# Optimization experiments

Hardware: AMD Instinct MI355X
Metric: run time of the kernel (lower is better)

The kernel has to match this reference:

```python
import jax, jax.numpy as jnp
import numpy as np

N, E, B, T = 50000, 800000, 256, 50
IN_DIM, H, C1, C2, Q_DIM, LH = 128, 4, 32, 128, 32, 128
EPS = 1e-5


def setup_inputs() -> dict:
    key = jax.random.key(0)
    ks = jax.random.split(key, 24)
    g = 0.05
    inp = {
        'x': jax.random.normal(ks[0], (N, IN_DIM), jnp.float32),
        'edge_index': jax.random.randint(ks[1], (2, E), 0, N, jnp.int32),
        'batch': jnp.sort(jax.random.randint(ks[2], (N,), 0, B, jnp.int32)),
        'quant': jax.random.normal(ks[3], (B, T, Q_DIM), jnp.float32),
        # GATConv(128 -> 32, heads=4, concat)
        'gat_W': jax.random.normal(ks[4], (IN_DIM, H * C1), jnp.float32) * g,
        'gat_att_src': jax.random.normal(ks[5], (H, C1), jnp.float32) * g,
        'gat_att_dst': jax.random.normal(ks[6], (H, C1), jnp.float32) * g,
        'gat_b': jnp.zeros((H * C1,), jnp.float32),
        # BN1 over 128 channels (eval mode)
        'bn1_gamma': jnp.ones((H * C1,), jnp.float32),
        'bn1_beta': jnp.zeros((H * C1,), jnp.float32),
        'bn1_mean': jax.random.normal(ks[7], (H * C1,), jnp.float32) * 0.01,
        'bn1_var': jnp.ones((H * C1,), jnp.float32),
        # GCNConv(128 -> 128)
        'gcn_W': jax.random.normal(ks[8], (H * C1, C2), jnp.float32) * g,
        'gcn_b': jnp.zeros((C2,), jnp.float32),
        'bn2_gamma': jnp.ones((C2,), jnp.float32),
        'bn2_beta': jnp.zeros((C2,), jnp.float32),
        'bn2_mean': jax.random.normal(ks[9], (C2,), jnp.float32) * 0.01,
        'bn2_var': jnp.ones((C2,), jnp.float32),
        # GlobalAttention gate: Linear(C2 -> 1)
        'gate_W': jax.random.normal(ks[10], (1, C2), jnp.float32) * g,
        'gate_b': jnp.zeros((1,), jnp.float32),
        # LSTM(Q_DIM -> LH), torch gate order i,f,g,o
        'lstm_Wih': jax.random.normal(ks[11], (4 * LH, Q_DIM), jnp.float32) * g,
        'lstm_Whh': jax.random.normal(ks[12], (4 * LH, LH), jnp.float32) * g,
        'lstm_bih': jnp.zeros((4 * LH,), jnp.float32),
        'lstm_bhh': jnp.zeros((4 * LH,), jnp.float32),
        # final Linear(C2+LH -> 1)
        'fc_W': jax.random.normal(ks[13], (1, C2 + LH), jnp.float32) * g,
        'fc_b': jnp.zeros((1,), jnp.float32),
    }
    return inp


def _segment_softmax(e, seg, num_segments):
    m = jax.ops.segment_max(e, seg, num_segments=num_segments)
    ex = jnp.exp(e - m[seg])
    s = jax.ops.segment_sum(ex, seg, num_segments=num_segments)
    return ex / (s[seg] + 1e-16)


def _bn_eval(x, gamma, beta, mean, var):
    return gamma * (x - mean) * jax.lax.rsqrt(var + EPS) + beta


def _forward(x, edge_index, batch, quant,
             gat_W, gat_att_src, gat_att_dst, gat_b,
             bn1_gamma, bn1_beta, bn1_mean, bn1_var,
             gcn_W, gcn_b, bn2_gamma, bn2_beta, bn2_mean, bn2_var,
             gate_W, gate_b,
             lstm_Wih, lstm_Whh, lstm_bih, lstm_bhh,
             fc_W, fc_b):
    n = x.shape[0]
    loops = jnp.arange(n, dtype=edge_index.dtype)
    ei = jnp.concatenate([edge_index, jnp.stack([loops, loops])], axis=1)  # add self loops
    src, dst = ei[0], ei[1]

    # ---- GATConv ----
    xw = (x @ gat_W).reshape(n, H, C1)                      # [N,H,C1]
    a_src = jnp.sum(xw * gat_att_src, axis=-1)              # [N,H]
    a_dst = jnp.sum(xw * gat_att_dst, axis=-1)
    e = jax.nn.leaky_relu(a_src[src] + a_dst[dst], 0.2)     # [E+N,H]
    alpha = _segment_softmax(e, dst, n)                     # softmax over in-edges per dst
    msg = xw[src] * alpha[:, :, None]                       # [E+N,H,C1]
    h = jax.ops.segment_sum(msg, dst, num_segments=n).reshape(n, H * C1) + gat_b

    h = jax.nn.elu(h)
    h = _bn_eval(h, bn1_gamma, bn1_beta, bn1_mean, bn1_var)

    # ---- GCNConv (sym-normalized with self loops) ----
    deg = jax.ops.segment_sum(jnp.ones_like(dst, jnp.float32), dst, num_segments=n)
    dinv = jnp.where(deg > 0, jax.lax.rsqrt(deg), 0.0)
    norm = dinv[src] * dinv[dst]                            # [E+N]
    hw = h @ gcn_W                                          # [N,C2]
    h2 = jax.ops.segment_sum(hw[src] * norm[:, None], dst, num_segments=n) + gcn_b

    h2 = jax.nn.elu(h2)
    h2 = _bn_eval(h2, bn2_gamma, bn2_beta, bn2_mean, bn2_var)

    # ---- GlobalAttention pooling over graphs ----
    gate = (h2 @ gate_W.T + gate_b)[:, 0]                   # [N]
    score = _segment_softmax(gate, batch, B)
    graph_rep = jax.ops.segment_sum(score[:, None] * h2, batch, num_segments=B)  # [B,C2]

    # ---- LSTM over quant series ----
    def step(carry, xt):
        hh, cc = carry
        gates = xt @ lstm_Wih.T + hh @ lstm_Whh.T + lstm_bih + lstm_bhh
        i, f, gg, o = jnp.split(gates, 4, axis=-1)
        cc = jax.nn.sigmoid(f) * cc + jax.nn.sigmoid(i) * jnp.tanh(gg)
        hh = jax.nn.sigmoid(o) * jnp.tanh(cc)
        return (hh, cc), None

    h0 = jnp.zeros((B, LH), quant.dtype)
    (hT, _), _ = jax.lax.scan(step, (h0, h0), jnp.swapaxes(quant, 0, 1))

    combined = jnp.concatenate([graph_rep, hT], axis=1)     # [B, C2+LH]
    out = (combined @ fc_W.T + fc_b)[:, 0]                  # [B]
    return out


def reference(x, edge_index, batch, quant,
              gat_W, gat_att_src, gat_att_dst, gat_b,
              bn1_gamma, bn1_beta, bn1_mean, bn1_var,
              gcn_W, gcn_b, bn2_gamma, bn2_beta, bn2_mean, bn2_var,
              gate_W, gate_b,
              lstm_Wih, lstm_Whh, lstm_bih, lstm_bhh,
              fc_W, fc_b):
    return _forward(x, edge_index, batch, quant,
                    gat_W, gat_att_src, gat_att_dst, gat_b,
                    bn1_gamma, bn1_beta, bn1_mean, bn1_var,
                    gcn_W, gcn_b, bn2_gamma, bn2_beta, bn2_mean, bn2_var,
                    gate_W, gate_b,
                    lstm_Wih, lstm_Whh, lstm_bih, lstm_bhh,
                    fc_W, fc_b)
```

## Files before the change

### kernel.cpp

```cpp
#include <hip/hip_runtime.h>
#include <cfloat>
#include <cstddef>

constexpr int KIN   = 128;
constexpr int KQD   = 32;
constexpr int KT    = 50;
constexpr int KLH   = 128;
constexpr float BN_EPS = 1e-5f;

typedef __attribute__((ext_vector_type(8))) short bf16x8;
typedef __attribute__((ext_vector_type(4))) float f32x4;
union U8 { bf16x8 v; unsigned u[4]; };

__device__ __forceinline__ float elu_f(float x)  { return x > 0.f ? x : expm1f(x); }
__device__ __forceinline__ float leaky_f(float x){ return x > 0.f ? x : 0.2f * x; }
__device__ __forceinline__ float fsigm(float x)  { return 1.f / (1.f + __expf(-x)); }
__device__ __forceinline__ float ftanh(float x)  { return 1.f - 2.f / (__expf(2.f * x) + 1.f); }

__device__ __forceinline__ unsigned bfpack(float lo, float hi) {
    unsigned ul = __float_as_uint(lo), uh = __float_as_uint(hi);
    ul += 0x7FFFu + ((ul >> 16) & 1u);
    uh += 0x7FFFu + ((uh >> 16) & 1u);
    return (ul >> 16) | (uh & 0xFFFF0000u);
}
__device__ __forceinline__ unsigned short bf1(float v) {
    unsigned u = __float_as_uint(v);
    u += 0x7FFFu + ((u >> 16) & 1u);
    return (unsigned short)(u >> 16);
}
__device__ __forceinline__ float bflo(unsigned u) { return __uint_as_float(u << 16); }
__device__ __forceinline__ float bfhi(unsigned u) { return __uint_as_float(u & 0xFFFF0000u); }

__device__ __forceinline__ bf16x8 pack8(float4 p, float4 q) {
    U8 t;
    t.u[0] = bfpack(p.x, p.y); t.u[1] = bfpack(p.z, p.w);
    t.u[2] = bfpack(q.x, q.y); t.u[3] = bfpack(q.z, q.w);
    return t.v;
}

__global__ void k_deg(const int* __restrict__ ei, int E, int* __restrict__ deg) {
    int e = blockIdx.x * blockDim.x + threadIdx.x;
    if (e < E) atomicAdd(&deg[ei[E + e]], 1);
}

__global__ __launch_bounds__(1024)
void k_scan_a(const int* __restrict__ deg, int n, int* __restrict__ bsum) {
    __shared__ int wsum[16];
    int tid = threadIdx.x, lane = tid & 63, w = tid >> 6;
    int i0 = blockIdx.x * 4096 + tid * 4;
    int t = 0;
    #pragma unroll
    for (int j = 0; j < 4; j++) t += (i0 + j < n) ? deg[i0 + j] : 0;
    #pragma unroll
    for (int d = 1; d < 64; d <<= 1) t += __shfl_xor(t, d);
    if (lane == 0) wsum[w] = t;
    __syncthreads();
    if (tid == 0) {
        int s = 0;
        #pragma unroll
        for (int k = 0; k < 16; k++) s += wsum[k];
        bsum[blockIdx.x] = s;
    }
}

__global__ void k_scan_b(int* __restrict__ bsum, int nb) {
    if (threadIdx.x == 0) {
        int run = 0;
        for (int i = 0; i < nb; i++) { int v = bsum[i]; bsum[i] = run; run += v; }
    }
}

__global__ __launch_bounds__(1024)
void k_scan_c(const int* __restrict__ deg, int n, const int* __restrict__ bsum,
              int* __restrict__ offsets, int* __restrict__ cursor,
              float* __restrict__ dinv) {
    __shared__ int wsum[16];
    int tid = threadIdx.x, lane = tid & 63, w = tid >> 6;
    int i0 = blockIdx.x * 4096 + tid * 4;
    int v[4];
    #pragma unroll
    for (int j = 0; j < 4; j++) v[j] = (i0 + j < n) ? deg[i0 + j] : 0;
    int tsum = v[0] + v[1] + v[2] + v[3];
    int sc = tsum;
    #pragma unroll
    for (int d = 1; d < 64; d <<= 1) {
        int o = __shfl_up(sc, d);
        if (lane >= d) sc += o;
    }
    if (lane == 63) wsum[w] = sc;
    __syncthreads();
    if (w == 0) {
        int xx = (lane < 16) ? wsum[lane] : 0;
        #pragma unroll
        for (int d = 1; d < 16; d <<= 1) {
            int o = __shfl_up(xx, d);
            if (lane >= d) xx += o;
        }
        if (lane < 16) wsum[lane] = xx;
    }
    __syncthreads();
    int run = bsum[blockIdx.x] + ((w > 0) ? wsum[w - 1] : 0) + sc - tsum;
    #pragma unroll
    for (int j = 0; j < 4; j++) {
        int i = i0 + j;
        if (i < n) {
            cursor[i]      = run;
            offsets[i + 1] = run + v[j];
            dinv[i]        = rsqrtf((float)(v[j] + 1));
            run += v[j];
        }
    }
    if (blockIdx.x == 0 && tid == 0) offsets[0] = 0;
}

__global__ void k_fill(const int* __restrict__ ei, int E, int* __restrict__ cursor,
                       int* __restrict__ csr_src) {
    int e = blockIdx.x * blockDim.x + threadIdx.x;
    if (e < E) {
        int s = ei[e], d = ei[E + e];
        int pos = atomicAdd(&cursor[d], 1);
        csr_src[pos] = s;
    }
}

template <bool ATT>
__global__ __launch_bounds__(256, 4)
void k_gemm_mfma(const float* __restrict__ X, const float* __restrict__ W,
                 unsigned* __restrict__ Yb, int nrows,
                 const float* __restrict__ attS, const float* __restrict__ attD,
                 float* __restrict__ a_src, float* __restrict__ a_dst) {
    __shared__ float tile[16][132];
    __shared__ float as_sh[128], ad_sh[128];
    int tid  = threadIdx.x;
    int lane = tid & 63;
    int wv   = tid >> 6;
    if (ATT && tid < 128) { as_sh[tid] = attS[tid]; ad_sh[tid] = attD[tid]; }
    int l16 = lane & 15;
    int kq  = (lane >> 4) * 8;
    bf16x8 bfr[2][4];
    #pragma unroll
    for (int nt = 0; nt < 2; nt++) {
        int n = wv * 32 + nt * 16 + l16;
        #pragma unroll
        for (int kk = 0; kk < 4; kk++) {
            int k0 = kk * 32 + kq;
            float f[8];
            #pragma unroll
            for (int j = 0; j < 8; j++) f[j] = W[(size_t)(k0 + j) * 128 + n];
            U8 t;
            t.u[0] = bfpack(f[0], f[1]); t.u[1] = bfpack(f[2], f[3]);
            t.u[2] = bfpack(f[4], f[5]); t.u[3] = bfpack(f[6], f[7]);
            bfr[nt][kk] = t.v;
        }
    }
    int nch = (nrows + 15) / 16;
    for (int ch = blockIdx.x; ch < nch; ch += gridDim.x) {
        int r0 = ch * 16;
        int r  = r0 + l16;
        bool rok = r < nrows;
        const float* xr = X + (size_t)r * 128 + kq;
        float4 z4 = make_float4(0.f, 0.f, 0.f, 0.f);
        bf16x8 afr[4];
        #pragma unroll
        for (int kk = 0; kk < 4; kk++) {
            float4 p = rok ? *reinterpret_cast<const float4*>(xr + kk * 32)     : z4;
            float4 q = rok ? *reinterpret_cast<const float4*>(xr + kk * 32 + 4) : z4;
            afr[kk] = pack8(p, q);
        }
        f32x4 acc0 = {0.f, 0.f, 0.f, 0.f};
        f32x4 acc1 = {0.f, 0.f, 0.f, 0.f};
        #pragma unroll
        for (int kk = 0; kk < 4; kk++) {
            acc0 = __builtin_amdgcn_mfma_f32_16x16x32_bf16(afr[kk], bfr[0][kk], acc0, 0, 0, 0);
            acc1 = __builtin_amdgcn_mfma_f32_16x16x32_bf16(afr[kk], bfr[1][kk], acc1, 0, 0, 0);
        }
        __syncthreads();
        int rowb = (lane >> 4) * 4;
        int cb   = wv * 32 + l16;
        #pragma unroll
        for (int reg = 0; reg < 4; reg++) {
            tile[rowb + reg][cb]      = acc0[reg];
            tile[rowb + reg][cb + 16] = acc1[reg];
        }
        __syncthreads();
        #pragma unroll
        for (int i = 0; i < 4; i++) {
            int idx = tid + i * 256;
            int row = idx >> 6, cp = idx & 63;
            int rr = r0 + row;
            if (rr < nrows) {
                float2 f = *reinterpret_cast<const float2*>(&tile[row][cp * 2]);
                Yb[(size_t)rr * 64 + cp] = bfpack(f.x, f.y);
            }
        }
        if (ATT && tid < 64) {
            int rr2 = tid >> 2, h = tid & 3;
            if (r0 + rr2 < nrows) {
                float ps = 0.f, pd = 0.f;
                #pragma unroll
                for (int j = 0; j < 32; j++) {
                    float v = tile[rr2][h * 32 + j];
                    ps += v * as_sh[h * 32 + j];
                    pd += v * ad_sh[h * 32 + j];
                }
                a_src[(size_t)(r0 + rr2) * 4 + h] = ps;
                a_dst[(size_t)(r0 + rr2) * 4 + h] = pd;
            }
        }
    }
}

__global__ __launch_bounds__(256)
void k_gat_agg(const int* __restrict__ offsets, const int* __restrict__ csr_src,
               const float* __restrict__ a_src, const float* __restrict__ a_dst,
               const unsigned* __restrict__ xwb, const float* __restrict__ bias,
               const float* __restrict__ g1, const float* __restrict__ b1,
               const float* __restrict__ mu1, const float* __restrict__ var1,
               float* __restrict__ hout, int n) {
    __shared__ int   src_sh[4][64];
    __shared__ float al_sh[4][4][64];
    int lane = threadIdx.x & 63;
    int wv   = threadIdx.x >> 6;
    int wid  = (blockIdx.x * blockDim.x + threadIdx.x) >> 6;
    int nw   = (gridDim.x * blockDim.x) >> 6;
    int hP   = lane >> 4;
    int c0 = lane * 2, c1 = c0 + 1;
    float bi0 = bias[c0], bi1 = bias[c1];
    float A0 = g1[c0] * rsqrtf(var1[c0] + BN_EPS);
    float A1 = g1[c1] * rsqrtf(var1[c1] + BN_EPS);
    float B0 = b1[c0] - mu1[c0] * A0;
    float B1 = b1[c1] - mu1[c1] * A1;
    for (int node = wid; node < n; node += nw) {
        int beg = offsets[node], end = offsets[node + 1];
        int rowlen = end - beg, total = rowlen + 1;
        float4 adv = *reinterpret_cast<const float4*>(&a_dst[(size_t)node * 4]);
        int sv = (lane < rowlen) ? csr_src[beg + lane] : node;
        float4 as4 = *reinterpret_cast<const float4*>(&a_src[(size_t)sv * 4]);
        float e0 = leaky_f(as4.x + adv.x), e1 = leaky_f(as4.y + adv.y);
        float e2 = leaky_f(as4.z + adv.z), e3 = leaky_f(as4.w + adv.w);
        float m[4] = {-FLT_MAX, -FLT_MAX, -FLT_MAX, -FLT_MAX};
        if (lane < total) { m[0] = e0; m[1] = e1; m[2] = e2; m[3] = e3; }
        for (int i = lane + 64; i < total; i += 64) {
            int src = (i < rowlen) ? csr_src[beg + i] : node;
            float4 a4 = *reinterpret_cast<const float4*>(&a_src[(size_t)src * 4]);
            m[0] = fmaxf(m[0], leaky_f(a4.x + adv.x));
            m[1] = fmaxf(m[1], leaky_f(a4.y + adv.y));
            m[2] = fmaxf(m[2], leaky_f(a4.z + adv.z));
            m[3] = fmaxf(m[3], leaky_f(a4.w + adv.w));
        }
        #pragma unroll
        for (int off = 32; off; off >>= 1) {
            #pragma unroll
            for (int h = 0; h < 4; h++) m[h] = fmaxf(m[h], __shfl_xor(m[h], off));
        }
        float ex[4] = {0.f, 0.f, 0.f, 0.f};
        if (lane < total) {
            ex[0] = expf(e0 - m[0]); ex[1] = expf(e1 - m[1]);
            ex[2] = expf(e2 - m[2]); ex[3] = expf(e3 - m[3]);
        }
        float s[4] = {ex[0], ex[1], ex[2], ex[3]};
        for (int i = lane + 64; i < total; i += 64) {
            int src = (i < rowlen) ? csr_src[beg + i] : node;
            float4 a4 = *reinterpret_cast<const float4*>(&a_src[(size_t)src * 4]);
            s[0] += expf(leaky_f(a4.x + adv.x) - m[0]);
            s[1] += expf(leaky_f(a4.y + adv.y) - m[1]);
            s[2] += expf(leaky_f(a4.z + adv.z) - m[2]);
            s[3] += expf(leaky_f(a4.w + adv.w) - m[3]);
        }
        #pragma unroll
        for (int off = 32; off; off >>= 1) {
            #pragma unroll
            for (int h = 0; h < 4; h++) s[h] += __shfl_xor(s[h], off);
        }
        float inv[4];
        #pragma unroll
        for (int h = 0; h < 4; h++) inv[h] = 1.f / (s[h] + 1e-16f);
        src_sh[wv][lane] = sv;
        #pragma unroll
        for (int h = 0; h < 4; h++) al_sh[wv][h][lane] = ex[h] * inv[h];
        __builtin_amdgcn_wave_barrier();
        float acc0 = 0.f, acc1 = 0.f;
        int cnt = min(total, 64);
        {
            int i = 0;
            for (; i + 4 <= cnt; i += 4) {
                int s0 = src_sh[wv][i],     s1 = src_sh[wv][i + 1];
                int s2 = src_sh[wv][i + 2], s3 = src_sh[wv][i + 3];
                float a0 = al_sh[wv][hP][i],     a1 = al_sh[wv][hP][i + 1];
                float a2 = al_sh[wv][hP][i + 2], a3 = al_sh[wv][hP][i + 3];
                unsigned u0 = xwb[(size_t)s0 * 64 + lane];
                unsigned u1 = xwb[(size_t)s1 * 64 + lane];
                unsigned u2 = xwb[(size_t)s2 * 64 + lane];
                unsigned u3 = xwb[(size_t)s3 * 64 + lane];
                acc0 += a0 * bflo(u0); acc1 += a0 * bfhi(u0);
                acc0 += a1 * bflo(u1); acc1 += a1 * bfhi(u1);
                acc0 += a2 * bflo(u2); acc1 += a2 * bfhi(u2);
                acc0 += a3 * bflo(u3); acc1 += a3 * bfhi(u3);
            }
            for (; i < cnt; i++) {
                int src  = src_sh[wv][i];
                float aP = al_sh[wv][hP][i];
                unsigned u = xwb[(size_t)src * 64 + lane];
                acc0 += aP * bflo(u);
                acc1 += aP * bfhi(u);
            }
        }
        for (int base = 64; base < total; base += 64) {
            __builtin_amdgcn_wave_barrier();
            int i = base + lane;
            int src2 = node;
            float a0v = 0.f, a1v = 0.f, a2v = 0.f, a3v = 0.f;
            if (i < total) {
                if (i < rowlen) src2 = csr_src[beg + i];
                float4 a4 = *reinterpret_cast<const float4*>(&a_src[(size_t)src2 * 4]);
                a0v = expf(leaky_f(a4.x + adv.x) - m[0]) * inv[0];
                a1v = expf(leaky_f(a4.y + adv.y) - m[1]) * inv[1];
                a2v = expf(leaky_f(a4.z + adv.z) - m[2]) * inv[2];
                a3v = expf(leaky_f(a4.w + adv.w) - m[3]) * inv[3];
            }
            src_sh[wv][lane] = src2;
            al_sh[wv][0][lane] = a0v; al_sh[wv][1][lane] = a1v;
            al_sh[wv][2][lane] = a2v; al_sh[wv][3][lane] = a3v;
            __builtin_amdgcn_wave_barrier();
            int cnt2 = min(total - base, 64);
            for (int j = 0; j < cnt2; j++) {
                int src  = src_sh[wv][j];
                float aP = al_sh[wv][hP][j];
                unsigned u = xwb[(size_t)src * 64 + lane];
                acc0 += aP * bflo(u);
                acc1 += aP * bfhi(u);
            }
        }
        __builtin_amdgcn_wave_barrier();
        float vA = elu_f(acc0 + bi0);
        float vB = elu_f(acc1 + bi1);
        vA = vA * A0 + B0;
        vB = vB * A1 + B1;
        *reinterpret_cast<float2*>(&hout[(size_t)node * 128 + c0]) =
            make_float2(vA, vB);
    }
}

__global__ __launch_bounds__(256)
void k_gcn_agg(const int* __restrict__ offsets, const int* __restrict__ csr_src,
               const float* __restrict__ dinv, const unsigned* __restrict__ hwb,
               const float* __restrict__ bias,
               const float* __restrict__ g2, const float* __restrict__ b2,
               const float* __restrict__ mu2, const float* __restrict__ var2,
               const float* __restrict__ gateW, const float* __restrict__ gateB,
               float* __restrict__ h2, float* __restrict__ gate, int n) {
    __shared__ int   src_sh[4][64];
    __shared__ float w_sh[4][64];
    int lane = threadIdx.x & 63;
    int wv   = threadIdx.x >> 6;
    int wid  = (blockIdx.x * blockDim.x + threadIdx.x) >> 6;
    int nw   = (gridDim.x * blockDim.x) >> 6;
    int c0 = lane * 2, c1 = c0 + 1;
    float bi0 = bias[c0], bi1 = bias[c1];
    float A0 = g2[c0] * rsqrtf(var2[c0] + BN_EPS);
    float A1 = g2[c1] * rsqrtf(var2[c1] + BN_EPS);
    float B0 = b2[c0] - mu2[c0] * A0;
    float B1 = b2[c1] - mu2[c1] * A1;
    float gw0 = gateW[c0], gw1 = gateW[c1], gB = gateB[0];
    for (int node = wid; node < n; node += nw) {
        int beg = offsets[node], end = offsets[node + 1];
        int rowlen = end - beg;
        float dn = dinv[node];
        unsigned us = hwb[(size_t)node * 64 + lane];
        float acc0 = dn * dn * bflo(us);
        float acc1 = dn * dn * bfhi(us);
        for (int base = 0; base < rowlen; base += 64) {
            __builtin_amdgcn_wave_barrier();
            int i = base + lane;
            int src2 = node;
            float wv2 = 0.f;
            if (i < rowlen) { src2 = csr_src[beg + i]; wv2 = dinv[src2] * dn; }
            src_sh[wv][lane] = src2;
            w_sh[wv][lane]   = wv2;
            __builtin_amdgcn_wave_barrier();
            int cnt = min(rowlen - base, 64);
            int j = 0;
            for (; j + 4 <= cnt; j += 4) {
                int s0 = src_sh[wv][j],     s1 = src_sh[wv][j + 1];
                int s2 = src_sh[wv][j + 2], s3 = src_sh[wv][j + 3];
                float w0 = w_sh[wv][j],     w1 = w_sh[wv][j + 1];
                float w2 = w_sh[wv][j + 2], w3 = w_sh[wv][j + 3];
                unsigned u0 = hwb[(size_t)s0 * 64 + lane];
                unsigned u1 = hwb[(size_t)s1 * 64 + lane];
                unsigned u2 = hwb[(size_t)s2 * 64 + lane];
                unsigned u3 = hwb[(size_t)s3 * 64 + lane];
                acc0 += w0 * bflo(u0); acc1 += w0 * bfhi(u0);
                acc0 += w1 * bflo(u1); acc1 += w1 * bfhi(u1);
                acc0 += w2 * bflo(u2); acc1 += w2 * bfhi(u2);
                acc0 += w3 * bflo(u3); acc1 += w3 * bfhi(u3);
            }
            for (; j < cnt; j++) {
                int src = src_sh[wv][j];
                float w = w_sh[wv][j];
                unsigned u = hwb[(size_t)src * 64 + lane];
                acc0 += w * bflo(u);
                acc1 += w * bfhi(u);
            }
        }
        __builtin_amdgcn_wave_barrier();
        float vA = elu_f(acc0 + bi0);
        float vB = elu_f(acc1 + bi1);
        vA = vA * A0 + B0;
        vB = vB * A1 + B1;
        *reinterpret_cast<float2*>(&h2[(size_t)node * 128 + c0]) =
            make_float2(vA, vB);
        float p = vA * gw0 + vB * gw1;
        #pragma unroll
        for (int off = 32; off; off >>= 1) p += __shfl_xor(p, off);
        if (lane == 0) gate[node] = p + gB;
    }
}

__device__ __forceinline__ int lbound(const int* a, int n, int key) {
    int lo = 0, hi = n;
    while (lo < hi) { int mid = (lo + hi) >> 1; if (a[mid] < key) lo = mid + 1; else hi = mid; }
    return lo;
}

__global__ __launch_bounds__(256)
void k_pool(const int* __restrict__ batch, const float* __restrict__ gate,
            const float* __restrict__ h2, const float* __restrict__ hT,
            const float* __restrict__ fcW, const float* __restrict__ fcB,
            float* __restrict__ out, int n) {
    int b = blockIdx.x, tid = threadIdx.x;
    __shared__ float red[256];
    __shared__ float sc_sh[256];
    int start = lbound(batch, n, b);
    int end   = lbound(batch, n, b + 1);
    float m = -FLT_MAX;
    for (int i = start + tid; i < end; i += 256) m = fmaxf(m, gate[i]);
    red[tid] = m; __syncthreads();
    for (int s2 = 128; s2 > 0; s2 >>= 1) {
        if (tid < s2) red[tid] = fmaxf(red[tid], red[tid + s2]);
        __syncthreads();
    }
    m = red[0]; __syncthreads();
    float s = 0.f;
    for (int i = start + tid; i < end; i += 256) s += expf(gate[i] - m);
    red[tid] = s; __syncthreads();
    for (int s2 = 128; s2 > 0; s2 >>= 1) {
        if (tid < s2) red[tid] += red[tid + s2];
        __syncthreads();
    }
    float inv = 1.f / (red[0] + 1e-16f);
    __syncthreads();
    int j = tid & 127, half = tid >> 7;
    float acc = 0.f;
    for (int base = start; base < end; base += 256) {
        int cnt = min(256, end - base);
        __syncthreads();
        if (tid < cnt) sc_sh[tid] = expf(gate[base + tid] - m) * inv;
        __syncthreads();
        for (int ii = half; ii < cnt; ii += 2)
            acc += sc_sh[ii] * h2[(size_t)(base + ii) * 128 + j];
    }
    red[tid] = acc; __syncthreads();
    if (half == 0) sc_sh[j] = red[j] + red[128 + j];
    __syncthreads();
    float p = 0.f;
    if (tid < 128)
        p = fcW[tid] * sc_sh[tid] + fcW[128 + tid] * hT[(size_t)b * 128 + tid];
    red[tid] = p; __syncthreads();
    for (int s2 = 128; s2 > 0; s2 >>= 1) {
        if (tid < s2) red[tid] += red[tid + s2];
        __syncthreads();
    }
    if (tid == 0) out[b] = red[0] + fcB[0];
}

__global__ __launch_bounds__(256)
void k_xproj(const float* __restrict__ quant, const float* __restrict__ Wih,
             const float* __restrict__ bih, const float* __restrict__ bhh,
             float* __restrict__ xproj) {
    int blk = blockIdx.x;
    int chunk = blk / KT, s = blk % KT;
    int lane = threadIdx.x & 63, w = threadIdx.x >> 6;
    int l15 = lane & 15, kq8 = (lane >> 4) * 8;
    int b = chunk * 16 + l15;
    const float* xr = &quant[(size_t)b * (KT * KQD) + s * KQD + kq8];
    bf16x8 ax = pack8(*reinterpret_cast<const float4*>(xr),
                      *reinterpret_cast<const float4*>(xr + 4));
    #pragma unroll
    for (int ti = 0; ti < 8; ti++) {
        int tc = w * 8 + ti;
        int gcol = w * 128 + ti * 16 + l15;
        const float* wr = &Wih[(size_t)gcol * KQD + kq8];
        bf16x8 bw = pack8(*reinterpret_cast<const float4*>(wr),
                          *reinterpret_cast<const float4*>(wr + 4));
        f32x4 acc = {0.f, 0.f, 0.f, 0.f};
        acc = __builtin_amdgcn_mfma_f32_16x16x32_bf16(ax, bw, acc, 0, 0, 0);
        float bv = bih[gcol] + bhh[gcol];
        acc[0] += bv; acc[1] += bv; acc[2] += bv; acc[3] += bv;
        *reinterpret_cast<f32x4*>(
            &xproj[(((size_t)chunk * KT + s) * 32 + tc) * 256 + lane * 4]) = acc;
    }
}

__global__ __launch_bounds__(512)
void k_lstm2(const float* __restrict__ xproj, const float* __restrict__ Whh,
             float* __restrict__ hstate) {
    __shared__ unsigned short h16[2][16][148];
    int t = threadIdx.x, lane = t & 63, w = t >> 6;
    int chunk = blockIdx.x;
    int l15 = lane & 15, kq8 = (lane >> 4) * 8;
    int j = w * 16 + l15;
    int rowq = (lane >> 4) * 4;
    bf16x8 whh_f[4][4];
    #pragma unroll
    for (int c = 0; c < 4; c++) {
        int col = c * 128 + j;
        #pragma unroll
        for (int kk = 0; kk < 4; kk++) {
            const float* wr = &Whh[(size_t)col * 128 + kk * 32 + kq8];
            whh_f[c][kk] = pack8(*reinterpret_cast<const float4*>(wr),
                                 *reinterpret_cast<const float4*>(wr + 4));
        }
    }
    for (int p = t; p < 16 * 148; p += 512) {
        int r = p / 148, cc = p - r * 148;
        h16[0][r][cc] = 0;
    }
    float cst[4] = {0.f, 0.f, 0.f, 0.f};
    const float* xb = xproj + ((size_t)chunk * KT) * 32 * 256;
    f32x4 xgA = *reinterpret_cast<const f32x4*>(&xb[(0 * 8 + w) * 256 + lane * 4]);
    f32x4 xgB = *reinterpret_cast<const f32x4*>(&xb[(1 * 8 + w) * 256 + lane * 4]);
    f32x4 xgC = *reinterpret_cast<const f32x4*>(&xb[(2 * 8 + w) * 256 + lane * 4]);
    f32x4 xgD = *reinterpret_cast<const f32x4*>(&xb[(3 * 8 + w) * 256 + lane * 4]);
    int cur = 0;
    __syncthreads();
    for (int s = 0; s < KT; s++) {
        f32x4 ai = xgA, af = xgB, ag = xgC, ao = xgD;
        #pragma unroll
        for (int kk = 0; kk < 4; kk++) {
            bf16x8 ah = *reinterpret_cast<const bf16x8*>(&h16[cur][l15][kk * 32 + kq8]);
            ai = __builtin_amdgcn_mfma_f32_16x16x32_bf16(ah, whh_f[0][kk], ai, 0, 0, 0);
            af = __builtin_amdgcn_mfma_f32_16x16x32_bf16(ah, whh_f[1][kk], af, 0, 0, 0);
            ag = __builtin_amdgcn_mfma_f32_16x16x32_bf16(ah, whh_f[2][kk], ag, 0, 0, 0);
            ao = __builtin_amdgcn_mfma_f32_16x16x32_bf16(ah, whh_f[3][kk], ao, 0, 0, 0);
        }
        if (s + 1 < KT) {
            const float* xs = &xb[((size_t)(s + 1) * 32 + w) * 256 + lane * 4];
            xgA = *reinterpret_cast<const f32x4*>(&xs[0 * 8 * 256]);
            xgB = *reinterpret_cast<const f32x4*>(&xs[1 * 8 * 256]);
            xgC = *reinterpret_cast<const f32x4*>(&xs[2 * 8 * 256]);
            xgD = *reinterpret_cast<const f32x4*>(&xs[3 * 8 * 256]);
        }
        int nxt = cur ^ 1;
        #pragma unroll
        for (int r = 0; r < 4; r++) {
            float ig = fsigm(ai[r]);
            float fg = fsigm(af[r]);
            float gg = ftanh(ag[r]);
            float og = fsigm(ao[r]);
            cst[r] = fg * cst[r] + ig * gg;
            h16[nxt][rowq + r][j] = bf1(og * ftanh(cst[r]));
        }
        __syncthreads();
        cur = nxt;
    }
    int b0 = chunk * 16;
    for (int p = t; p < 16 * KLH; p += 512) {
        int row = p >> 7, jj = p & 127;
        hstate[(size_t)(b0 + row) * KLH + jj] =
            __uint_as_float((unsigned)h16[cur][row][jj] << 16);
    }
}

extern "C" void kernel_launch(void* const* d_in, const int* in_sizes, int n_in,
                              void* d_out, int out_size, void* d_ws, size_t ws_size,
                              hipStream_t stream) {
    const float* x     = (const float*)d_in[0];
    const int*   ei    = (const int*)  d_in[1];
    const int*   batch = (const int*)  d_in[2];
    const float* quant = (const float*)d_in[3];
    const float* gatW  = (const float*)d_in[4];
    const float* attS  = (const float*)d_in[5];
    const float* attD  = (const float*)d_in[6];
    const float* gatB  = (const float*)d_in[7];
    const float* bn1g  = (const float*)d_in[8];
    const float* bn1b  = (const float*)d_in[9];
    const float* bn1m  = (const float*)d_in[10];
    const float* bn1v  = (const float*)d_in[11];
    const float* gcnW  = (const float*)d_in[12];
    const float* gcnB  = (const float*)d_in[13];
    const float* bn2g  = (const float*)d_in[14];
    const float* bn2b  = (const float*)d_in[15];
    const float* bn2m  = (const float*)d_in[16];
    const float* bn2v  = (const float*)d_in[17];
    const float* gateW = (const float*)d_in[18];
    const float* gateB = (const float*)d_in[19];
    const float* Wih   = (const float*)d_in[20];
    const float* Whh   = (const float*)d_in[21];
    const float* bih   = (const float*)d_in[22];
    const float* bhh   = (const float*)d_in[23];
    const float* fcW   = (const float*)d_in[24];
    const float* fcB   = (const float*)d_in[25];

    int N = in_sizes[0] / KIN;
    int E = in_sizes[1] / 2;
    int B = in_sizes[3] / (KT * KQD);
    int nchunks = B / 16;

    char* ws = (char*)d_ws;
    size_t off = 0;
    auto alloc = [&](size_t bytes) -> void* {
        void* p = ws + off;
        off += (bytes + 511) & ~(size_t)511;
        return p;
    };
    int nb = (N + 4095) / 4096;
    int*      deg     = (int*)     alloc((size_t)N * 4);
    int*      offsets = (int*)     alloc((size_t)(N + 1) * 4);
    int*      cursor  = (int*)     alloc((size_t)N * 4);
    float*    dinv    = (float*)   alloc((size_t)N * 4);
    int*      csr_src = (int*)     alloc((size_t)E * 4);
    int*      bsum    = (int*)     alloc((size_t)nb * 4);
    float*    a_src   = (float*)   alloc((size_t)N * 16);
    float*    a_dst   = (float*)   alloc((size_t)N * 16);
    unsigned* xwb     = (unsigned*)alloc((size_t)N * 256);
    float*    hbuf    = (float*)   alloc((size_t)N * 512);
    float*    gate    = (float*)   alloc((size_t)N * 4);
    float*    hstate  = (float*)   alloc((size_t)B * KLH * 4);
    float*    xproj   = (float*)   alloc((size_t)nchunks * KT * 32 * 256 * 4);

    hipMemsetAsync(deg, 0, (size_t)N * 4, stream);
    int eb = (E + 255) / 256;
    k_deg   <<<eb, 256, 0, stream>>>(ei, E, deg);
    k_scan_a<<<nb, 1024, 0, stream>>>(deg, N, bsum);
    k_scan_b<<<1, 64, 0, stream>>>(bsum, nb);
    k_scan_c<<<nb, 1024, 0, stream>>>(deg, N, bsum, offsets, cursor, dinv);
    k_fill  <<<eb, 256, 0, stream>>>(ei, E, cursor, csr_src);

    k_xproj<<<nchunks * KT, 256, 0, stream>>>(quant, Wih, bih, bhh, xproj);
    k_lstm2<<<nchunks, 512, 0, stream>>>(xproj, Whh, hstate);

    k_gemm_mfma<true ><<<512, 256, 0, stream>>>(x, gatW, xwb, N, attS, attD, a_src, a_dst);
    k_gat_agg<<<3072, 256, 0, stream>>>(offsets, csr_src, a_src, a_dst, xwb, gatB,
                                        bn1g, bn1b, bn1m, bn1v, hbuf, N);
    k_gemm_mfma<false><<<512, 256, 0, stream>>>(hbuf, gcnW, xwb, N,
                                                nullptr, nullptr, nullptr, nullptr);
    k_gcn_agg<<<3072, 256, 0, stream>>>(offsets, csr_src, dinv, xwb, gcnB,
                                        bn2g, bn2b, bn2m, bn2v, gateW, gateB,
                                        hbuf, gate, N);
    k_pool<<<B, 256, 0, stream>>>(batch, gate, hbuf, hstate, fcW, fcB,
                                  (float*)d_out, N);
}
```

Measured before the change: 432.1 us.

## Use fast exp intrinsics, unroll gathers by 8, restructure LSTM gate math, widen GEMM grid

Replaces expf/expm1f with __expf throughout the GAT softmax, pooling and ELU. The neighbour-gather loops in the GAT and GCN aggregation are unrolled from 4 to 8 to expose more independent loads. The LSTM step now prefetches the next step's input projection before the MFMAs and computes the gate nonlinearities with fewer divisions, using combined exponentials and hardware reciprocals. The GEMM launch grids are doubled from 512 to 1024 blocks. Fast exp and rcp lower accuracy slightly, and the 8-way unroll raises register pressure.

```diff
diff --git a/kernel.cpp b/kernel.cpp
--- a/kernel.cpp
+++ b/kernel.cpp
@@ -12,10 +12,8 @@
 typedef __attribute__((ext_vector_type(4))) float f32x4;
 union U8 { bf16x8 v; unsigned u[4]; };
 
-__device__ __forceinline__ float elu_f(float x)  { return x > 0.f ? x : expm1f(x); }
+__device__ __forceinline__ float elu_f(float x)  { return x > 0.f ? x : (__expf(x) - 1.f); }
 __device__ __forceinline__ float leaky_f(float x){ return x > 0.f ? x : 0.2f * x; }
-__device__ __forceinline__ float fsigm(float x)  { return 1.f / (1.f + __expf(-x)); }
-__device__ __forceinline__ float ftanh(float x)  { return 1.f - 2.f / (__expf(2.f * x) + 1.f); }
 
 __device__ __forceinline__ unsigned bfpack(float lo, float hi) {
     unsigned ul = __float_as_uint(lo), uh = __float_as_uint(hi);
@@ -255,17 +253,17 @@
         }
         float ex[4] = {0.f, 0.f, 0.f, 0.f};
         if (lane < total) {
-            ex[0] = expf(e0 - m[0]); ex[1] = expf(e1 - m[1]);
-            ex[2] = expf(e2 - m[2]); ex[3] = expf(e3 - m[3]);
+            ex[0] = __expf(e0 - m[0]); ex[1] = __expf(e1 - m[1]);
+            ex[2] = __expf(e2 - m[2]); ex[3] = __expf(e3 - m[3]);
         }
         float s[4] = {ex[0], ex[1], ex[2], ex[3]};
         for (int i = lane + 64; i < total; i += 64) {
             int src = (i < rowlen) ? csr_src[beg + i] : node;
             float4 a4 = *reinterpret_cast<const float4*>(&a_src[(size_t)src * 4]);
-            s[0] += expf(leaky_f(a4.x + adv.x) - m[0]);
-            s[1] += expf(leaky_f(a4.y + adv.y) - m[1]);
-            s[2] += expf(leaky_f(a4.z + adv.z) - m[2]);
-            s[3] += expf(leaky_f(a4.w + adv.w) - m[3]);
+            s[0] += __expf(leaky_f(a4.x + adv.x) - m[0]);
+            s[1] += __expf(leaky_f(a4.y + adv.y) - m[1]);
+            s[2] += __expf(leaky_f(a4.z + adv.z) - m[2]);
+            s[3] += __expf(leaky_f(a4.w + adv.w) - m[3]);
         }
         #pragma unroll
         for (int off = 32; off; off >>= 1) {
@@ -283,19 +281,14 @@
         int cnt = min(total, 64);
         {
             int i = 0;
-            for (; i + 4 <= cnt; i += 4) {
-                int s0 = src_sh[wv][i],     s1 = src_sh[wv][i + 1];
-                int s2 = src_sh[wv][i + 2], s3 = src_sh[wv][i + 3];
-                float a0 = al_sh[wv][hP][i],     a1 = al_sh[wv][hP][i + 1];
-                float a2 = al_sh[wv][hP][i + 2], a3 = al_sh[wv][hP][i + 3];
-                unsigned u0 = xwb[(size_t)s0 * 64 + lane];
-                unsigned u1 = xwb[(size_t)s1 * 64 + lane];
-                unsigned u2 = xwb[(size_t)s2 * 64 + lane];
-                unsigned u3 = xwb[(size_t)s3 * 64 + lane];
-                acc0 += a0 * bflo(u0); acc1 += a0 * bfhi(u0);
-                acc0 += a1 * bflo(u1); acc1 += a1 * bfhi(u1);
-                acc0 += a2 * bflo(u2); acc1 += a2 * bfhi(u2);
-                acc0 += a3 * bflo(u3); acc1 += a3 * bfhi(u3);
+            for (; i + 8 <= cnt; i += 8) {
+                int   sj[8]; float aj[8]; unsigned uj[8];
+                #pragma unroll
+                for (int q = 0; q < 8; q++) { sj[q] = src_sh[wv][i + q]; aj[q] = al_sh[wv][hP][i + q]; }
+                #pragma unroll
+                for (int q = 0; q < 8; q++) uj[q] = xwb[(size_t)sj[q] * 64 + lane];
+                #pragma unroll
+                for (int q = 0; q < 8; q++) { acc0 += aj[q] * bflo(uj[q]); acc1 += aj[q] * bfhi(uj[q]); }
             }
             for (; i < cnt; i++) {
                 int src  = src_sh[wv][i];
@@ -313,10 +306,10 @@
             if (i < total) {
                 if (i < rowlen) src2 = csr_src[beg + i];
                 float4 a4 = *reinterpret_cast<const float4*>(&a_src[(size_t)src2 * 4]);
-                a0v = expf(leaky_f(a4.x + adv.x) - m[0]) * inv[0];
-                a1v = expf(leaky_f(a4.y + adv.y) - m[1]) * inv[1];
-                a2v = expf(leaky_f(a4.z + adv.z) - m[2]) * inv[2];
-                a3v = expf(leaky_f(a4.w + adv.w) - m[3]) * inv[3];
+                a0v = __expf(leaky_f(a4.x + adv.x) - m[0]) * inv[0];
+                a1v = __expf(leaky_f(a4.y + adv.y) - m[1]) * inv[1];
+                a2v = __expf(leaky_f(a4.z + adv.z) - m[2]) * inv[2];
+                a3v = __expf(leaky_f(a4.w + adv.w) - m[3]) * inv[3];
             }
             src_sh[wv][lane] = src2;
             al_sh[wv][0][lane] = a0v; al_sh[wv][1][lane] = a1v;
@@ -380,19 +373,14 @@
             __builtin_amdgcn_wave_barrier();
             int cnt = min(rowlen - base, 64);
             int j = 0;
-            for (; j + 4 <= cnt; j += 4) {
-                int s0 = src_sh[wv][j],     s1 = src_sh[wv][j + 1];
-                int s2 = src_sh[wv][j + 2], s3 = src_sh[wv][j + 3];
-                float w0 = w_sh[wv][j],     w1 = w_sh[wv][j + 1];
-                float w2 = w_sh[wv][j + 2], w3 = w_sh[wv][j + 3];
-                unsigned u0 = hwb[(size_t)s0 * 64 + lane];
-                unsigned u1 = hwb[(size_t)s1 * 64 + lane];
-                unsigned u2 = hwb[(size_t)s2 * 64 + lane];
-                unsigned u3 = hwb[(size_t)s3 * 64 + lane];
-                acc0 += w0 * bflo(u0); acc1 += w0 * bfhi(u0);
-                acc0 += w1 * bflo(u1); acc1 += w1 * bfhi(u1);
-                acc0 += w2 * bflo(u2); acc1 += w2 * bfhi(u2);
-                acc0 += w3 * bflo(u3); acc1 += w3 * bfhi(u3);
+            for (; j + 8 <= cnt; j += 8) {
+                int   sj[8]; float wj[8]; unsigned uj[8];
+                #pragma unroll
+                for (int q = 0; q < 8; q++) { sj[q] = src_sh[wv][j + q]; wj[q] = w_sh[wv][j + q]; }
+                #pragma unroll
+                for (int q = 0; q < 8; q++) uj[q] = hwb[(size_t)sj[q] * 64 + lane];
+                #pragma unroll
+                for (int q = 0; q < 8; q++) { acc0 += wj[q] * bflo(uj[q]); acc1 += wj[q] * bfhi(uj[q]); }
             }
             for (; j < cnt; j++) {
                 int src = src_sh[wv][j];
@@ -441,7 +429,7 @@
     }
     m = red[0]; __syncthreads();
     float s = 0.f;
-    for (int i = start + tid; i < end; i += 256) s += expf(gate[i] - m);
+    for (int i = start + tid; i < end; i += 256) s += __expf(gate[i] - m);
     red[tid] = s; __syncthreads();
     for (int s2 = 128; s2 > 0; s2 >>= 1) {
         if (tid < s2) red[tid] += red[tid + s2];
@@ -454,7 +442,7 @@
     for (int base = start; base < end; base += 256) {
         int cnt = min(256, end - base);
         __syncthreads();
-        if (tid < cnt) sc_sh[tid] = expf(gate[base + tid] - m) * inv;
+        if (tid < cnt) sc_sh[tid] = __expf(gate[base + tid] - m) * inv;
         __syncthreads();
         for (int ii = half; ii < cnt; ii += 2)
             acc += sc_sh[ii] * h2[(size_t)(base + ii) * 128 + j];
@@ -534,6 +522,14 @@
     int cur = 0;
     __syncthreads();
     for (int s = 0; s < KT; s++) {
+        f32x4 nA, nB, nC, nD;
+        if (s + 1 < KT) {
+            const float* xs = &xb[((size_t)(s + 1) * 32 + w) * 256 + lane * 4];
+            nA = *reinterpret_cast<const f32x4*>(&xs[0 * 8 * 256]);
+            nB = *reinterpret_cast<const f32x4*>(&xs[1 * 8 * 256]);
+            nC = *reinterpret_cast<const f32x4*>(&xs[2 * 8 * 256]);
+            nD = *reinterpret_cast<const f32x4*>(&xs[3 * 8 * 256]);
+        }
         f32x4 ai = xgA, af = xgB, ag = xgC, ao = xgD;
         #pragma unroll
         for (int kk = 0; kk < 4; kk++) {
@@ -543,23 +539,25 @@
             ag = __builtin_amdgcn_mfma_f32_16x16x32_bf16(ah, whh_f[2][kk], ag, 0, 0, 0);
             ao = __builtin_amdgcn_mfma_f32_16x16x32_bf16(ah, whh_f[3][kk], ao, 0, 0, 0);
         }
-        if (s + 1 < KT) {
-            const float* xs = &xb[((size_t)(s + 1) * 32 + w) * 256 + lane * 4];
-            xgA = *reinterpret_cast<const f32x4*>(&xs[0 * 8 * 256]);
-            xgB = *reinterpret_cast<const f32x4*>(&xs[1 * 8 * 256]);
-            xgC = *reinterpret_cast<const f32x4*>(&xs[2 * 8 * 256]);
-            xgD = *reinterpret_cast<const f32x4*>(&xs[3 * 8 * 256]);
-        }
         int nxt = cur ^ 1;
         #pragma unroll
         for (int r = 0; r < 4; r++) {
-            float ig = fsigm(ai[r]);
-            float fg = fsigm(af[r]);
-            float gg = ftanh(ag[r]);
-            float og = fsigm(ao[r]);
-            cst[r] = fg * cst[r] + ig * gg;
-            h16[nxt][rowq + r][j] = bf1(og * ftanh(cst[r]));
-        }
+            float eiv = __expf(fminf(-ai[r], 25.f));
+            float efv = __expf(fminf(-af[r], 25.f));
+            float egv = __expf(fminf(2.f * ag[r], 50.f));
+            float eov = __expf(fminf(-ao[r], 25.f));
+            float pi = 1.f + eiv, pf = 1.f + efv;
+            float gp = egv + 1.f, gm = egv - 1.f;
+            float P  = pi * gp;
+            float D  = pf * P;
+            float cn = fmaf(cst[r], P, gm * pf) * __builtin_amdgcn_rcpf(D);
+            cst[r] = cn;
+            float ecv = __expf(fminf(2.f * cn, 50.f));
+            float D2  = (1.f + eov) * (ecv + 1.f);
+            float hv  = (ecv - 1.f) * __builtin_amdgcn_rcpf(D2);
+            h16[nxt][rowq + r][j] = bf1(hv);
+        }
+        xgA = nA; xgB = nB; xgC = nC; xgD = nD;
         __syncthreads();
         cur = nxt;
     }
@@ -639,11 +637,11 @@
     k_xproj<<<nchunks * KT, 256, 0, stream>>>(quant, Wih, bih, bhh, xproj);
     k_lstm2<<<nchunks, 512, 0, stream>>>(xproj, Whh, hstate);
 
-    k_gemm_mfma<true ><<<512, 256, 0, stream>>>(x, gatW, xwb, N, attS, attD, a_src, a_dst);
+    k_gemm_mfma<true ><<<1024, 256, 0, stream>>>(x, gatW, xwb, N, attS, attD, a_src, a_dst);
     k_gat_agg<<<3072, 256, 0, stream>>>(offsets, csr_src, a_src, a_dst, xwb, gatB,
                                         bn1g, bn1b, bn1m, bn1v, hbuf, N);
-    k_gemm_mfma<false><<<512, 256, 0, stream>>>(hbuf, gcnW, xwb, N,
-                                                nullptr, nullptr, nullptr, nullptr);
+    k_gemm_mfma<false><<<1024, 256, 0, stream>>>(hbuf, gcnW, xwb, N,
+                                                 nullptr, nullptr, nullptr, nullptr);
     k_gcn_agg<<<3072, 256, 0, stream>>>(offsets, csr_src, dinv, xwb, gcnB,
                                         bn2g, bn2b, bn2m, bn2v, gateW, gateB,
                                         hbuf, gate, N);
```

After: 409.4 us. 5.3% less time.
